# Performance work log

Hardware: AMD Instinct MI355X
Metric: run time of the kernel (lower is better)

## Reference

```python
import jax, jax.numpy as jnp
import numpy as np
import math

B, S, H = 4, 1024, 768
NH, DH = 12, 64
POS = 2 * S
INIT_STD = 0.02


def rel_shift_bnij(x, klen):
    # x: [b, n, i, j] -> Transformer-XL relative shift
    b, n, i, j = x.shape
    x = x.reshape(b, n, j, i)
    x = x[:, :, 1:, :]
    x = x.reshape(b, n, i, j - 1)
    return x[:, :, :, :klen]


def setup_inputs() -> dict:
    key = jax.random.key(0)
    ks = jax.random.split(key, 10)
    hidden = jax.random.normal(ks[0], (B, S, H), dtype=jnp.float32)
    pos_emb = jax.random.normal(ks[1], (B, POS, H), dtype=jnp.float32)
    mask = (jax.random.uniform(ks[2], (B, S, S)) < 0.1).astype(jnp.float32)
    q = INIT_STD * jax.random.normal(ks[3], (H, NH, DH), dtype=jnp.float32)
    kv = INIT_STD * jax.random.normal(ks[4], (H, NH, DH), dtype=jnp.float32)
    r = INIT_STD * jax.random.normal(ks[5], (H, NH, DH), dtype=jnp.float32)
    r_r_bias = INIT_STD * jax.random.normal(ks[6], (NH, DH), dtype=jnp.float32)
    r_w_bias = INIT_STD * jax.random.normal(ks[7], (NH, DH), dtype=jnp.float32)
    w_out = INIT_STD * jax.random.normal(ks[8], (NH * DH, H), dtype=jnp.float32)
    b_out = jnp.zeros((H,), dtype=jnp.float32)
    return {"hidden": hidden, "pos_emb": pos_emb, "mask": mask,
            "q": q, "kv": kv, "r": r,
            "r_r_bias": r_r_bias, "r_w_bias": r_w_bias,
            "w_out": w_out, "b_out": b_out}


def reference(hidden, pos_emb, mask, q, kv, r, r_r_bias, r_w_bias, w_out, b_out):
    b, s, dim = hidden.shape
    d_head = q.shape[-1]
    q_head_h = jnp.einsum('bih,hnd->bind', hidden, q)
    kv_head_h = jnp.einsum('bih,hnd->bind', hidden, kv)
    k_head_r = jnp.einsum('bih,hnd->bind', pos_emb, r)
    # content and position score terms
    ac = jnp.einsum('bind,bjnd->bnij', q_head_h + r_w_bias, kv_head_h)
    bd = jnp.einsum('bind,bjnd->bnij', q_head_h + r_r_bias, k_head_r)
    bd = rel_shift_bnij(bd, klen=ac.shape[3])
    scores = (ac + bd) / math.sqrt(d_head)
    scores = scores + mask[:, None, :, :] * (-65500.0)
    alpha = jax.nn.softmax(scores, axis=-1)  # dropout is identity in eval
    res = jnp.einsum('bhmn,bnhd->bmhd', alpha, kv_head_h).reshape(b, s, dim)
    res = res @ w_out + b_out
    res = hidden + res  # graph_residual=True
    return jax.nn.gelu(res, approximate=False)
```

## Files before the change

kernel.cpp:

```cpp
#include <hip/hip_runtime.h>

typedef unsigned short u16;
typedef unsigned int u32;
typedef unsigned long long u64;
typedef __attribute__((ext_vector_type(8))) short bf8v;
typedef __attribute__((ext_vector_type(4))) float f32x4;
typedef __attribute__((ext_vector_type(4))) u32 u32x4;
typedef __attribute__((ext_vector_type(2))) __fp16 fp16x2;

#define S_   1024
#define POS_ 2048

__device__ __forceinline__ float b2f(u16 h){
  union { float f; unsigned u; } x; x.u = ((unsigned)h) << 16; return x.f;
}
__device__ __forceinline__ u16 f2b(float f){
  union { float f; unsigned u; } x; x.f = f;
  unsigned u = x.u;
  return (u16)((u + 0x7fffu + ((u >> 16) & 1u)) >> 16);
}
__device__ __forceinline__ u16 f2bt(float f){
  union { float f; unsigned u; } x; x.f = f;
  return (u16)(x.u >> 16);
}

#define GLDS16(g, l) __builtin_amdgcn_global_load_lds( \
    (const __attribute__((address_space(1))) unsigned int*)(g), \
    (__attribute__((address_space(3))) unsigned int*)(l), 16, 0, 0)

__global__ __launch_bounds__(256) void prep(const float* __restrict__ q, const float* __restrict__ kv,
                                            const float* __restrict__ r, const float* __restrict__ wo,
                                            u16* __restrict__ wqkv, u16* __restrict__ wout,
                                            const float* __restrict__ mask, u32* __restrict__ mbT,
                                            u16* __restrict__ zp,
                                            const float* __restrict__ hidden, const float* __restrict__ pos,
                                            u16* __restrict__ hb, u16* __restrict__ pb){
  int blk = blockIdx.x, tid = threadIdx.x;
  if (blk < 2304){
    __shared__ u16 t[32][33];
    int z = blk / 576, rem = blk % 576;
    const float* src; u16* dst;
    if (z == 0){ src = q;  dst = wqkv; }
    else if (z == 1){ src = kv; dst = wqkv + 768*768; }
    else if (z == 2){ src = r;  dst = wqkv + 2*768*768; }
    else { src = wo; dst = wout; }
    int gx = (rem % 24)*32, gy = (rem / 24)*32;
    int tx = tid & 31, ty = tid >> 5;
    #pragma unroll
    for (int k = 0; k < 4; ++k)
      t[ty + 8*k][tx] = f2b(src[(gy + ty + 8*k)*768 + gx + tx]);
    __syncthreads();
    #pragma unroll
    for (int k = 0; k < 4; ++k)
      dst[(gx + ty + 8*k)*768 + gy + tx] = t[tx][ty + 8*k];
  } else if (blk < 2816){
    int widx = (blk - 2304)*4 + (tid >> 6);
    int lane = tid & 63;
    int kt = widx & 15, bi = widx >> 4;
    const float* mrow = mask + (size_t)bi*32*1024 + kt*64 + lane;
    u32 m = 0;
    #pragma unroll
    for (int rr = 0; rr < 32; ++rr)
      m |= (mrow[(size_t)rr*1024] != 0.0f ? 1u : 0u) << rr;
    mbT[(size_t)widx*64 + lane] = m;
    if (blk == 2304 && tid < 8) zp[tid] = 0;
  } else {
    size_t i = ((size_t)(blk - 2816)*256 + tid)*8;
    const float* s; u16* d;
    if (i < 3145728){ s = hidden + i; d = hb + i; }
    else { s = pos + (i - 3145728); d = pb + (i - 3145728); }
    f32x4 x0 = *(const f32x4*)s, x1 = *(const f32x4*)(s + 4);
    bf8v t;
    #pragma unroll
    for (int j = 0; j < 4; ++j){ t[j] = f2b(x0[j]); t[4+j] = f2b(x1[j]); }
    *(bf8v*)d = t;
  }
}

template<int MODE>
__device__ __forceinline__ void gemm_core(const void* Av, int lda, const u16* Bt,
                                          u16* Cv, int ldc,
                                          int bm, int bn,
                                          u16 (*As)[32], u16 (*Bs)[32]){
  int tid = threadIdx.x;
  int lane = tid & 63, rg = tid >> 6;
  int quad = lane >> 4, l15 = lane & 15;
  int wm = rg >> 1, wn = rg & 1;
  int poff = (quad ^ ((l15 >> 1) & 3)) * 8;
  f32x4 acc[4][4];
  #pragma unroll
  for (int i = 0; i < 4; ++i)
    #pragma unroll
    for (int j = 0; j < 4; ++j)
      acc[i][j] = (f32x4){0.f,0.f,0.f,0.f};

  for (int kt = 0; kt < 24; ++kt){
    int k0 = kt*32;
    if (kt) __syncthreads();
    #pragma unroll
    for (int t = 0; t < 2; ++t){
      int m = (rg*2 + t)*16 + (lane >> 2);
      int g = ((lane & 3) ^ ((m >> 1) & 3)) * 8;
      GLDS16(&Bt[(size_t)(bn*128 + m)*768 + k0 + g], &Bs[m][(lane & 3)*8]);
    }
    if (MODE & 2){
      #pragma unroll
      for (int t = 0; t < 2; ++t){
        int m = (rg*2 + t)*16 + (lane >> 2);
        int g = ((lane & 3) ^ ((m >> 1) & 3)) * 8;
        GLDS16(&((const u16*)Av)[(size_t)(bm*128 + m)*lda + k0 + g], &As[m][(lane & 3)*8]);
      }
    } else {
      #pragma unroll
      for (int e = 0; e < 2; ++e){
        int v = tid + 256*e;
        int m = v >> 2, c = v & 3;
        const u32* ap = (const u32*)Av + (size_t)(bm*128 + m)*lda + k0 + c*8;
        u32x4 a0 = *(const u32x4*)ap;
        u32x4 a1 = *(const u32x4*)(ap + 4);
        u32x4 pk;
        pk[0] = (a0[0] >> 16) | (a0[1] & 0xFFFF0000u);
        pk[1] = (a0[2] >> 16) | (a0[3] & 0xFFFF0000u);
        pk[2] = (a1[0] >> 16) | (a1[1] & 0xFFFF0000u);
        pk[3] = (a1[2] >> 16) | (a1[3] & 0xFFFF0000u);
        *(u32x4*)&As[m][(c ^ ((m >> 1) & 3))*8] = pk;
      }
    }
    __syncthreads();
    bf8v af[4], bf[4];
    #pragma unroll
    for (int mt = 0; mt < 4; ++mt) af[mt] = *(const bf8v*)&As[wm*64 + mt*16 + l15][poff];
    #pragma unroll
    for (int nt = 0; nt < 4; ++nt) bf[nt] = *(const bf8v*)&Bs[wn*64 + nt*16 + l15][poff];
    #pragma unroll
    for (int mt = 0; mt < 4; ++mt)
      #pragma unroll
      for (int nt = 0; nt < 4; ++nt)
        acc[mt][nt] = __builtin_amdgcn_mfma_f32_16x16x32_bf16(af[mt], bf[nt], acc[mt][nt], 0, 0, 0);
  }

  #pragma unroll
  for (int mt = 0; mt < 4; ++mt)
    #pragma unroll
    for (int nt = 0; nt < 4; ++nt)
      #pragma unroll
      for (int reg = 0; reg < 4; ++reg){
        int grow = bm*128 + wm*64 + mt*16 + quad*4 + reg;
        int gcol = bn*128 + wn*64 + nt*16 + l15;
        Cv[(size_t)grow*ldc + gcol] = f2b(acc[mt][nt][reg]);
      }
}

__global__ __launch_bounds__(256) void gemm_proj(const void* __restrict__ A1, const void* __restrict__ A2,
                                                 const u16* __restrict__ wqkv,
                                                 u16* __restrict__ qkvh, u16* __restrict__ krh, int amode){
  __shared__ u16 As[128][32];
  __shared__ u16 Bs[128][32];
  int t = blockIdx.x;
  if (t < 384){
    if (amode) gemm_core<2>(A1, 768, wqkv, qkvh, 1536, t & 31, t >> 5, As, Bs);
    else       gemm_core<0>(A1, 768, wqkv, qkvh, 1536, t & 31, t >> 5, As, Bs);
  } else {
    t -= 384;
    if (amode) gemm_core<2>(A2, 768, wqkv + 2*768*768, krh, 768, t & 63, t >> 6, As, Bs);
    else       gemm_core<0>(A2, 768, wqkv + 2*768*768, krh, 768, t & 63, t >> 6, As, Bs);
  }
}

__global__ __launch_bounds__(256) void gemm_out(const u16* __restrict__ ctx, const u16* __restrict__ wout,
                                                float* __restrict__ out,
                                                const float* __restrict__ resid, const float* __restrict__ bias){
  __shared__ u16 As[64][32];
  __shared__ u16 Bs[64][32];
  int tid = threadIdx.x;
  int lane = tid & 63, rg = tid >> 6;
  int quad = lane >> 4, l15 = lane & 15;
  int wm = rg >> 1, wn = rg & 1;
  int bm = blockIdx.x, bn = blockIdx.y;
  f32x4 acc[2][2];
  #pragma unroll
  for (int i = 0; i < 2; ++i)
    #pragma unroll
    for (int j = 0; j < 2; ++j)
      acc[i][j] = (f32x4){0.f,0.f,0.f,0.f};

  int m = tid >> 2, s = (tid & 3)*8;
  for (int kt = 0; kt < 24; ++kt){
    int k0 = kt*32;
    if (kt) __syncthreads();
    GLDS16(&ctx[(size_t)(bm*64 + m)*768 + k0 + s], &As[m][s]);
    GLDS16(&wout[(size_t)(bn*64 + m)*768 + k0 + s], &Bs[m][s]);
    __syncthreads();
    bf8v af[2], bf[2];
    #pragma unroll
    for (int mt = 0; mt < 2; ++mt) af[mt] = *(const bf8v*)&As[wm*32 + mt*16 + l15][quad*8];
    #pragma unroll
    for (int nt = 0; nt < 2; ++nt) bf[nt] = *(const bf8v*)&Bs[wn*32 + nt*16 + l15][quad*8];
    #pragma unroll
    for (int mt = 0; mt < 2; ++mt)
      #pragma unroll
      for (int nt = 0; nt < 2; ++nt)
        acc[mt][nt] = __builtin_amdgcn_mfma_f32_16x16x32_bf16(af[mt], bf[nt], acc[mt][nt], 0, 0, 0);
  }

  #pragma unroll
  for (int mt = 0; mt < 2; ++mt)
    #pragma unroll
    for (int nt = 0; nt < 2; ++nt)
      #pragma unroll
      for (int reg = 0; reg < 4; ++reg){
        int grow = bm*64 + wm*32 + mt*16 + quad*4 + reg;
        int gcol = bn*64 + wn*32 + nt*16 + l15;
        float v = acc[mt][nt][reg] + bias[gcol] + resid[(size_t)grow*768 + gcol];
        v = 0.5f * v * (1.0f + erff(v * 0.70710678118654752f));
        out[(size_t)grow*768 + gcol] = v;
      }
}

__global__ __launch_bounds__(256, 4) void attn(const u16* __restrict__ qkvh,
                                               const u16* __restrict__ krh,
                                               const u32* __restrict__ mbT,
                                               const float* __restrict__ rrb,
                                               const float* __restrict__ rwb,
                                               const u16* __restrict__ zp,
                                               u16* __restrict__ ctx){
  __shared__ u16 kvL[64][64];
  __shared__ u16 krL[96][64];
  __shared__ u16 pL[32][72];
  __shared__ float lpart[4][32];

  int tid = threadIdx.x;
  int lane = tid & 63, w = tid >> 6;
  int quad = lane >> 4, l15 = lane & 15;

  int fid = blockIdx.x;
  int xcd = fid & 7, loc = fid >> 3;
  int pair = xcd*6 + (loc >> 5);
  int i0 = (loc & 31) * 32;
  int b = pair / 12, n = pair % 12;

  const u16* kvbase = qkvh + (size_t)b*S_*1536 + 768 + n*64;
  const u16* krbase = krh + (size_t)b*POS_*768 + n*64;
  const float SC = 0.18033688f;

  bf8v qwf[2][2], qrf[2][2];
  #pragma unroll
  for (int rgi = 0; rgi < 2; ++rgi)
    #pragma unroll
    for (int c = 0; c < 2; ++c){
      int d0 = c*32 + quad*8;
      bf8v qv = *(const bf8v*)&qkvh[(size_t)(b*S_ + i0 + rgi*16 + l15)*1536 + n*64 + d0];
      f32x4 w0 = *(const f32x4*)&rwb[n*64 + d0];
      f32x4 w1 = *(const f32x4*)&rwb[n*64 + d0 + 4];
      f32x4 r0 = *(const f32x4*)&rrb[n*64 + d0];
      f32x4 r1 = *(const f32x4*)&rrb[n*64 + d0 + 4];
      bf8v qw, qr;
      #pragma unroll
      for (int j = 0; j < 4; ++j){
        float qf0 = b2f((u16)qv[j]), qf1 = b2f((u16)qv[4+j]);
        qw[j]   = f2b((qf0 + w0[j])*SC);
        qw[4+j] = f2b((qf1 + w1[j])*SC);
        qr[j]   = f2b((qf0 + r0[j])*SC);
        qr[4+j] = f2b((qf1 + r1[j])*SC);
      }
      qwf[rgi][c] = qw;
      qrf[rgi][c] = qr;
    }

  f32x4 ctxa[2];
  float l_acc[2][4];
  #pragma unroll
  for (int i = 0; i < 2; ++i){
    ctxa[i] = (f32x4){0.f,0.f,0.f,0.f};
    #pragma unroll
    for (int j = 0; j < 4; ++j) l_acc[i][j] = 0.f;
  }

  int key = w*16 + l15;
  int pvcol = (((key >> 3) + 2*quad) & 7)*8 + (key & 7);
  int cswz = ((l15 >> 2) & 3) << 3;
  const u32* mrowp = mbT + ((size_t)(b*32 + (i0 >> 5))*16)*64 + key;

  for (int kt = 0; kt < 16; ++kt){
    int k0 = kt*64;
    int j0 = k0 + S_ - i0 - 31;
    __syncthreads();
    #pragma unroll
    for (int e = 0; e < 2; ++e){
      int v = tid + 256*e;
      int k = v >> 3, s = v & 7;
      int g = (s - 2*(k >> 3)) & 7;
      GLDS16(&kvbase[(size_t)(k0 + k)*1536 + g*8], &kvL[k][s*8]);
    }
    #pragma unroll
    for (int e = 0; e < 3; ++e){
      int v = tid + 256*e;
      int jj = v >> 3, s = v & 7;
      int g = (s - 3*(jj >> 3)) & 7;
      int jg = j0 + jj;
      const u16* src = (jg < POS_) ? &krbase[(size_t)jg*768 + g*8] : zp;
      GLDS16(src, &krL[jj][s*8]);
    }
    u32 mrow = mrowp[(size_t)kt*64];
    __syncthreads();

    int rA = w*16 + l15;
    f32x4 ac0 = (f32x4){0.f,0.f,0.f,0.f}, ac1 = (f32x4){0.f,0.f,0.f,0.f};
    f32x4 b00 = (f32x4){0.f,0.f,0.f,0.f}, b01 = (f32x4){0.f,0.f,0.f,0.f};
    f32x4 b10 = (f32x4){0.f,0.f,0.f,0.f}, b11 = (f32x4){0.f,0.f,0.f,0.f};
    #pragma unroll
    for (int c = 0; c < 2; ++c){
      int p = (c*4 + quad + 2*(key >> 3)) & 7;
      bf8v bkv = *(const bf8v*)&kvL[key][p*8];
      ac0 = __builtin_amdgcn_mfma_f32_16x16x32_bf16(qwf[0][c], bkv, ac0, 0, 0, 0);
      ac1 = __builtin_amdgcn_mfma_f32_16x16x32_bf16(qwf[1][c], bkv, ac1, 0, 0, 0);
    }
    #pragma unroll
    for (int c = 0; c < 2; ++c){
      int rB = rA + 16;
      bf8v kB = *(const bf8v*)&krL[rB][((c*4 + quad + 3*(rB >> 3)) & 7)*8];
      b00 = __builtin_amdgcn_mfma_f32_16x16x32_bf16(qrf[0][c], kB, b00, 0, 0, 0);
      b11 = __builtin_amdgcn_mfma_f32_16x16x32_bf16(qrf[1][c], kB, b11, 0, 0, 0);
    }
    #pragma unroll
    for (int c = 0; c < 2; ++c){
      int rC = rA + 32;
      bf8v kC = *(const bf8v*)&krL[rC][((c*4 + quad + 3*(rC >> 3)) & 7)*8];
      b01 = __builtin_amdgcn_mfma_f32_16x16x32_bf16(qrf[0][c], kC, b01, 0, 0, 0);
    }
    #pragma unroll
    for (int c = 0; c < 2; ++c){
      bf8v kA = *(const bf8v*)&krL[rA][((c*4 + quad + 3*(rA >> 3)) & 7)*8];
      b10 = __builtin_amdgcn_mfma_f32_16x16x32_bf16(qrf[1][c], kA, b10, 0, 0, 0);
    }

    f32x4 acA[2]  = {ac0, ac1};
    f32x4 bdLo[2] = {b00, b10};
    f32x4 bdHi[2] = {b01, b11};
    #pragma unroll
    for (int rgi = 0; rgi < 2; ++rgi){
      u32 mq = mrow >> (rgi*16 + quad*4);
      u32 pk_[4];
      #pragma unroll
      for (int reg = 0; reg < 4; ++reg){
        union { fp16x2 h; u32 u; } cv;
        cv.h = __builtin_amdgcn_cvt_pkrtz(bdLo[rgi][reg], bdHi[rgi][reg]);
        pk_[reg] = cv.u;
      }
      #pragma unroll
      for (int reg = 0; reg < 4; ++reg){
        int sj = l15 + 15 - (quad*4 + reg);
        int srcl = (sj & 15) | (lane & 48);
        u32 got = (u32)__builtin_amdgcn_ds_bpermute(srcl << 2, (int)pk_[reg]);
        union { u16 s; __fp16 h; } hv;
        hv.s = (u16)(got >> (sj & 16));
        float sc = acA[rgi][reg] + (float)hv.h;
        float e = exp2f(sc);
        float p = ((mq >> reg) & 1u) ? 0.0f : e;
        l_acc[rgi][reg] += p;
        pL[rgi*16 + quad*4 + reg][key ^ (quad << 3)] = f2bt(p);
      }
    }
    __syncthreads();

    bf8v bv[2];
    #pragma unroll
    for (int c = 0; c < 2; ++c)
      #pragma unroll
      for (int j = 0; j < 8; ++j)
        bv[c][j] = (short)kvL[c*32 + quad*8 + j][pvcol];
    #pragma unroll
    for (int rgi = 0; rgi < 2; ++rgi)
      #pragma unroll
      for (int c = 0; c < 2; ++c){
        bf8v pa = *(const bf8v*)&pL[rgi*16 + l15][c*32 + ((quad*8) ^ cswz)];
        ctxa[rgi] = __builtin_amdgcn_mfma_f32_16x16x32_bf16(pa, bv[c], ctxa[rgi], 0, 0, 0);
      }
  }

  #pragma unroll
  for (int rgi = 0; rgi < 2; ++rgi)
    #pragma unroll
    for (int reg = 0; reg < 4; ++reg){
      float v = l_acc[rgi][reg];
      #pragma unroll
      for (int off = 1; off < 16; off <<= 1) v += __shfl_xor(v, off);
      l_acc[rgi][reg] = v;
    }
  if (l15 == 0){
    #pragma unroll
    for (int rgi = 0; rgi < 2; ++rgi)
      #pragma unroll
      for (int reg = 0; reg < 4; ++reg)
        lpart[w][rgi*16 + quad*4 + reg] = l_acc[rgi][reg];
  }
  __syncthreads();
  #pragma unroll
  for (int rgi = 0; rgi < 2; ++rgi)
    #pragma unroll
    for (int reg = 0; reg < 4; ++reg){
      int rloc = rgi*16 + quad*4 + reg;
      float lt = lpart[0][rloc] + lpart[1][rloc] + lpart[2][rloc] + lpart[3][rloc];
      ctx[(size_t)(b*S_ + i0 + rloc)*768 + n*64 + w*16 + l15] = f2b(ctxa[rgi][reg] / lt);
    }
}

extern "C" void kernel_launch(void* const* d_in, const int* in_sizes, int n_in,
                              void* d_out, int out_size, void* d_ws, size_t ws_size,
                              hipStream_t stream){
  (void)in_sizes; (void)n_in; (void)out_size;
  const float* hidden = (const float*)d_in[0];
  const float* pos    = (const float*)d_in[1];
  const float* maskp  = (const float*)d_in[2];
  const float* q      = (const float*)d_in[3];
  const float* kv     = (const float*)d_in[4];
  const float* r      = (const float*)d_in[5];
  const float* rrb    = (const float*)d_in[6];
  const float* rwb    = (const float*)d_in[7];
  const float* wo     = (const float*)d_in[8];
  const float* bo     = (const float*)d_in[9];
  float* out = (float*)d_out;

  u16* qkvh = (u16*)d_ws;
  u16* krh  = qkvh + (size_t)4096*1536;
  u16* wout = krh  + (size_t)8192*768;
  u16* wqkv = wout + 768*768;
  bool big = ws_size >= 49283104ull;
  u16 *hb = nullptr, *pb = nullptr, *ctx;
  u64* mbp;
  if (big){
    hb  = wqkv + (size_t)3*768*768;
    pb  = hb + (size_t)4096*768;
    ctx = hb;
    mbp = (u64*)(pb + (size_t)8192*768);
  } else {
    ctx = wqkv;
    mbp = (u64*)(wqkv + (size_t)4096*768);
  }
  u16* zp = (u16*)(mbp + 65536);

  prep<<<dim3(big ? 7424 : 2816), 256, 0, stream>>>(q, kv, r, wo, wqkv, wout,
                                                    maskp, (u32*)mbp, zp, hidden, pos, hb, pb);
  if (big) gemm_proj<<<dim3(768), 256, 0, stream>>>(hb, pb, wqkv, qkvh, krh, 2);
  else     gemm_proj<<<dim3(768), 256, 0, stream>>>(hidden, pos, wqkv, qkvh, krh, 0);
  attn<<<dim3(1536), 256, 0, stream>>>(qkvh, krh, (const u32*)mbp, rrb, rwb, zp, ctx);
  gemm_out<<<dim3(64,12), 256, 0, stream>>>(ctx, wout, out, hidden, bo);
}
```

Before: 219.5 us.

## Double GEMM K-tile to 64 with XOR swizzle, move mask packing into projection

The projection and output GEMMs now use a K step of 64 instead of 32, which halves the number of K iterations and barriers. Both use a wider 8-way XOR swizzle to avoid LDS bank conflicts, and the output GEMM gains a swizzle it lacked before. Mask bit-packing moves from the prep kernel into extra blocks of the projection kernel so it overlaps with the GEMM work. The cost is doubled LDS per block (32 KB for the projection), which may lower occupancy.

```diff
diff --git a/kernel.cpp b/kernel.cpp
--- a/kernel.cpp
+++ b/kernel.cpp
@@ -31,8 +31,6 @@
 __global__ __launch_bounds__(256) void prep(const float* __restrict__ q, const float* __restrict__ kv,
                                             const float* __restrict__ r, const float* __restrict__ wo,
                                             u16* __restrict__ wqkv, u16* __restrict__ wout,
-                                            const float* __restrict__ mask, u32* __restrict__ mbT,
-                                            u16* __restrict__ zp,
                                             const float* __restrict__ hidden, const float* __restrict__ pos,
                                             u16* __restrict__ hb, u16* __restrict__ pb){
   int blk = blockIdx.x, tid = threadIdx.x;
@@ -53,19 +51,8 @@
     #pragma unroll
     for (int k = 0; k < 4; ++k)
       dst[(gx + ty + 8*k)*768 + gy + tx] = t[tx][ty + 8*k];
-  } else if (blk < 2816){
-    int widx = (blk - 2304)*4 + (tid >> 6);
-    int lane = tid & 63;
-    int kt = widx & 15, bi = widx >> 4;
-    const float* mrow = mask + (size_t)bi*32*1024 + kt*64 + lane;
-    u32 m = 0;
-    #pragma unroll
-    for (int rr = 0; rr < 32; ++rr)
-      m |= (mrow[(size_t)rr*1024] != 0.0f ? 1u : 0u) << rr;
-    mbT[(size_t)widx*64 + lane] = m;
-    if (blk == 2304 && tid < 8) zp[tid] = 0;
   } else {
-    size_t i = ((size_t)(blk - 2816)*256 + tid)*8;
+    size_t i = ((size_t)(blk - 2304)*256 + tid)*8;
     const float* s; u16* d;
     if (i < 3145728){ s = hidden + i; d = hb + i; }
     else { s = pos + (i - 3145728); d = pb + (i - 3145728); }
@@ -81,12 +68,11 @@
 __device__ __forceinline__ void gemm_core(const void* Av, int lda, const u16* Bt,
                                           u16* Cv, int ldc,
                                           int bm, int bn,
-                                          u16 (*As)[32], u16 (*Bs)[32]){
+                                          u16 (*As)[64], u16 (*Bs)[64]){
   int tid = threadIdx.x;
   int lane = tid & 63, rg = tid >> 6;
   int quad = lane >> 4, l15 = lane & 15;
   int wm = rg >> 1, wn = rg & 1;
-  int poff = (quad ^ ((l15 >> 1) & 3)) * 8;
   f32x4 acc[4][4];
   #pragma unroll
   for (int i = 0; i < 4; ++i)
@@ -94,27 +80,29 @@
     for (int j = 0; j < 4; ++j)
       acc[i][j] = (f32x4){0.f,0.f,0.f,0.f};
 
-  for (int kt = 0; kt < 24; ++kt){
-    int k0 = kt*32;
+  for (int kt = 0; kt < 12; ++kt){
+    int k0 = kt*64;
     if (kt) __syncthreads();
     #pragma unroll
-    for (int t = 0; t < 2; ++t){
-      int m = (rg*2 + t)*16 + (lane >> 2);
-      int g = ((lane & 3) ^ ((m >> 1) & 3)) * 8;
-      GLDS16(&Bt[(size_t)(bn*128 + m)*768 + k0 + g], &Bs[m][(lane & 3)*8]);
+    for (int e = 0; e < 4; ++e){
+      int v = tid + 256*e;
+      int m = v >> 3, s = v & 7;
+      int g = s ^ ((m >> 1) & 7);
+      GLDS16(&Bt[(size_t)(bn*128 + m)*768 + k0 + g*8], &Bs[m][s*8]);
     }
     if (MODE & 2){
       #pragma unroll
-      for (int t = 0; t < 2; ++t){
-        int m = (rg*2 + t)*16 + (lane >> 2);
-        int g = ((lane & 3) ^ ((m >> 1) & 3)) * 8;
-        GLDS16(&((const u16*)Av)[(size_t)(bm*128 + m)*lda + k0 + g], &As[m][(lane & 3)*8]);
+      for (int e = 0; e < 4; ++e){
+        int v = tid + 256*e;
+        int m = v >> 3, s = v & 7;
+        int g = s ^ ((m >> 1) & 7);
+        GLDS16(&((const u16*)Av)[(size_t)(bm*128 + m)*lda + k0 + g*8], &As[m][s*8]);
       }
     } else {
       #pragma unroll
-      for (int e = 0; e < 2; ++e){
+      for (int e = 0; e < 4; ++e){
         int v = tid + 256*e;
-        int m = v >> 2, c = v & 3;
+        int m = v >> 3, c = v & 7;
         const u32* ap = (const u32*)Av + (size_t)(bm*128 + m)*lda + k0 + c*8;
         u32x4 a0 = *(const u32x4*)ap;
         u32x4 a1 = *(const u32x4*)(ap + 4);
@@ -123,20 +111,31 @@
         pk[1] = (a0[2] >> 16) | (a0[3] & 0xFFFF0000u);
         pk[2] = (a1[0] >> 16) | (a1[1] & 0xFFFF0000u);
         pk[3] = (a1[2] >> 16) | (a1[3] & 0xFFFF0000u);
-        *(u32x4*)&As[m][(c ^ ((m >> 1) & 3))*8] = pk;
-      }
-    }
-    __syncthreads();
-    bf8v af[4], bf[4];
-    #pragma unroll
-    for (int mt = 0; mt < 4; ++mt) af[mt] = *(const bf8v*)&As[wm*64 + mt*16 + l15][poff];
-    #pragma unroll
-    for (int nt = 0; nt < 4; ++nt) bf[nt] = *(const bf8v*)&Bs[wn*64 + nt*16 + l15][poff];
-    #pragma unroll
-    for (int mt = 0; mt < 4; ++mt)
-      #pragma unroll
-      for (int nt = 0; nt < 4; ++nt)
-        acc[mt][nt] = __builtin_amdgcn_mfma_f32_16x16x32_bf16(af[mt], bf[nt], acc[mt][nt], 0, 0, 0);
+        *(u32x4*)&As[m][(c ^ ((m >> 1) & 7))*8] = pk;
+      }
+    }
+    __syncthreads();
+    #pragma unroll
+    for (int kc = 0; kc < 2; ++kc){
+      bf8v af[4], bf[4];
+      #pragma unroll
+      for (int mt = 0; mt < 4; ++mt){
+        int mrow = wm*64 + mt*16 + l15;
+        int p = (kc*4 + quad) ^ ((mrow >> 1) & 7);
+        af[mt] = *(const bf8v*)&As[mrow][p*8];
+      }
+      #pragma unroll
+      for (int nt = 0; nt < 4; ++nt){
+        int nrow = wn*64 + nt*16 + l15;
+        int p = (kc*4 + quad) ^ ((nrow >> 1) & 7);
+        bf[nt] = *(const bf8v*)&Bs[nrow][p*8];
+      }
+      #pragma unroll
+      for (int mt = 0; mt < 4; ++mt)
+        #pragma unroll
+        for (int nt = 0; nt < 4; ++nt)
+          acc[mt][nt] = __builtin_amdgcn_mfma_f32_16x16x32_bf16(af[mt], bf[nt], acc[mt][nt], 0, 0, 0);
+    }
   }
 
   #pragma unroll
@@ -153,10 +152,26 @@
 
 __global__ __launch_bounds__(256) void gemm_proj(const void* __restrict__ A1, const void* __restrict__ A2,
                                                  const u16* __restrict__ wqkv,
-                                                 u16* __restrict__ qkvh, u16* __restrict__ krh, int amode){
-  __shared__ u16 As[128][32];
-  __shared__ u16 Bs[128][32];
+                                                 u16* __restrict__ qkvh, u16* __restrict__ krh,
+                                                 const float* __restrict__ mask, u32* __restrict__ mbT,
+                                                 u16* __restrict__ zp, int amode){
+  __shared__ u16 As[128][64];
+  __shared__ u16 Bs[128][64];
   int t = blockIdx.x;
+  if (t >= 768){
+    int tid = threadIdx.x;
+    int widx = (t - 768)*4 + (tid >> 6);
+    int lane = tid & 63;
+    int kt = widx & 15, bi = widx >> 4;
+    const float* mrow = mask + (size_t)bi*32*1024 + kt*64 + lane;
+    u32 m = 0;
+    #pragma unroll
+    for (int rr = 0; rr < 32; ++rr)
+      m |= (mrow[(size_t)rr*1024] != 0.0f ? 1u : 0u) << rr;
+    mbT[(size_t)widx*64 + lane] = m;
+    if (t == 768 && tid < 8) zp[tid] = 0;
+    return;
+  }
   if (t < 384){
     if (amode) gemm_core<2>(A1, 768, wqkv, qkvh, 1536, t & 31, t >> 5, As, Bs);
     else       gemm_core<0>(A1, 768, wqkv, qkvh, 1536, t & 31, t >> 5, As, Bs);
@@ -170,8 +185,8 @@
 __global__ __launch_bounds__(256) void gemm_out(const u16* __restrict__ ctx, const u16* __restrict__ wout,
                                                 float* __restrict__ out,
                                                 const float* __restrict__ resid, const float* __restrict__ bias){
-  __shared__ u16 As[64][32];
-  __shared__ u16 Bs[64][32];
+  __shared__ u16 As[64][64];
+  __shared__ u16 Bs[64][64];
   int tid = threadIdx.x;
   int lane = tid & 63, rg = tid >> 6;
   int quad = lane >> 4, l15 = lane & 15;
@@ -184,23 +199,39 @@
     for (int j = 0; j < 2; ++j)
       acc[i][j] = (f32x4){0.f,0.f,0.f,0.f};
 
-  int m = tid >> 2, s = (tid & 3)*8;
-  for (int kt = 0; kt < 24; ++kt){
-    int k0 = kt*32;
+  for (int kt = 0; kt < 12; ++kt){
+    int k0 = kt*64;
     if (kt) __syncthreads();
-    GLDS16(&ctx[(size_t)(bm*64 + m)*768 + k0 + s], &As[m][s]);
-    GLDS16(&wout[(size_t)(bn*64 + m)*768 + k0 + s], &Bs[m][s]);
-    __syncthreads();
-    bf8v af[2], bf[2];
-    #pragma unroll
-    for (int mt = 0; mt < 2; ++mt) af[mt] = *(const bf8v*)&As[wm*32 + mt*16 + l15][quad*8];
-    #pragma unroll
-    for (int nt = 0; nt < 2; ++nt) bf[nt] = *(const bf8v*)&Bs[wn*32 + nt*16 + l15][quad*8];
-    #pragma unroll
-    for (int mt = 0; mt < 2; ++mt)
-      #pragma unroll
-      for (int nt = 0; nt < 2; ++nt)
-        acc[mt][nt] = __builtin_amdgcn_mfma_f32_16x16x32_bf16(af[mt], bf[nt], acc[mt][nt], 0, 0, 0);
+    #pragma unroll
+    for (int e = 0; e < 2; ++e){
+      int v = tid + 256*e;
+      int m = v >> 3, s = v & 7;
+      int g = s ^ ((m >> 1) & 7);
+      GLDS16(&ctx[(size_t)(bm*64 + m)*768 + k0 + g*8], &As[m][s*8]);
+      GLDS16(&wout[(size_t)(bn*64 + m)*768 + k0 + g*8], &Bs[m][s*8]);
+    }
+    __syncthreads();
+    #pragma unroll
+    for (int kc = 0; kc < 2; ++kc){
+      bf8v af[2], bf[2];
+      #pragma unroll
+      for (int mt = 0; mt < 2; ++mt){
+        int mrow = wm*32 + mt*16 + l15;
+        int p = (kc*4 + quad) ^ ((mrow >> 1) & 7);
+        af[mt] = *(const bf8v*)&As[mrow][p*8];
+      }
+      #pragma unroll
+      for (int nt = 0; nt < 2; ++nt){
+        int nrow = wn*32 + nt*16 + l15;
+        int p = (kc*4 + quad) ^ ((nrow >> 1) & 7);
+        bf[nt] = *(const bf8v*)&Bs[nrow][p*8];
+      }
+      #pragma unroll
+      for (int mt = 0; mt < 2; ++mt)
+        #pragma unroll
+        for (int nt = 0; nt < 2; ++nt)
+          acc[mt][nt] = __builtin_amdgcn_mfma_f32_16x16x32_bf16(af[mt], bf[nt], acc[mt][nt], 0, 0, 0);
+    }
   }
 
   #pragma unroll
@@ -439,10 +470,11 @@
   }
   u16* zp = (u16*)(mbp + 65536);
 
-  prep<<<dim3(big ? 7424 : 2816), 256, 0, stream>>>(q, kv, r, wo, wqkv, wout,
-                                                    maskp, (u32*)mbp, zp, hidden, pos, hb, pb);
-  if (big) gemm_proj<<<dim3(768), 256, 0, stream>>>(hb, pb, wqkv, qkvh, krh, 2);
-  else     gemm_proj<<<dim3(768), 256, 0, stream>>>(hidden, pos, wqkv, qkvh, krh, 0);
+  prep<<<dim3(big ? 6912 : 2304), 256, 0, stream>>>(q, kv, r, wo, wqkv, wout, hidden, pos, hb, pb);
+  if (big) gemm_proj<<<dim3(1280), 256, 0, stream>>>(hb, pb, wqkv, qkvh, krh,
+                                                     maskp, (u32*)mbp, zp, 2);
+  else     gemm_proj<<<dim3(1280), 256, 0, stream>>>(hidden, pos, wqkv, qkvh, krh,
+                                                     maskp, (u32*)mbp, zp, 0);
   attn<<<dim3(1536), 256, 0, stream>>>(qkvh, krh, (const u32*)mbp, rrb, rwb, zp, ctx);
   gemm_out<<<dim3(64,12), 256, 0, stream>>>(ctx, wout, out, hidden, bo);
 }
```

Measured after the change: 223.8 us. Within noise of the previous version (+1.9%).
